# Kernel tuning notes

Hardware: AMD Instinct MI355X
Metric: run time of the kernel (lower is better)

## Reference

```python
import jax, jax.numpy as jnp
import numpy as np
import math

B, C, H, W = 4, 256, 64, 64
DQK = max(1, C // 8)  # 32


def setup_inputs() -> dict:
    key = jax.random.key(0)
    ks = jax.random.split(key, 6)
    x = jax.random.normal(ks[0], (B, C, H, W), dtype=jnp.float32)
    Wq = jax.random.normal(ks[1], (DQK, C), dtype=jnp.float32) * (1.0 / math.sqrt(C))
    bq = jnp.zeros((DQK,), dtype=jnp.float32)
    Wk = jax.random.normal(ks[2], (DQK, C), dtype=jnp.float32) * (1.0 / math.sqrt(C))
    bk = jnp.zeros((DQK,), dtype=jnp.float32)
    Wv = jax.random.normal(ks[3], (C, C), dtype=jnp.float32) * (1.0 / math.sqrt(C))
    bv = jnp.zeros((C,), dtype=jnp.float32)
    gamma = jax.random.normal(ks[4], (1,), dtype=jnp.float32)
    return {"x": x, "Wq": Wq, "bq": bq, "Wk": Wk, "bk": bk, "Wv": Wv, "bv": bv, "gamma": gamma}


def reference(x, Wq, bq, Wk, bk, Wv, bv, gamma):
    b, c, h, w = x.shape
    n = h * w
    xf = x.reshape(b, c, n)                                  # [B, C, N]
    # 1x1 convs == per-pixel linear projections
    q = jnp.einsum('bcn,dc->bdn', xf, Wq) + bq[None, :, None]  # [B, DQK, N]
    k = jnp.einsum('bcn,dc->bdn', xf, Wk) + bk[None, :, None]  # [B, DQK, N]
    v = jnp.einsum('bcn,oc->bon', xf, Wv) + bv[None, :, None]  # [B, C, N]
    scale = 1.0 / math.sqrt(q.shape[1] + 1e-8)
    attn = jnp.einsum('bdi,bdj->bij', q, k) * scale            # [B, N, N]
    attn = jax.nn.softmax(attn, axis=-1)
    out = jnp.einsum('bcj,bij->bci', v, attn)                  # [B, C, N]
    out = out.reshape(b, c, h, w)
    return gamma[0] * out + x
```

## Files before the change

kernel.cpp:

```cpp
#include <hip/hip_runtime.h>
#include <hip/hip_bf16.h>
#include <math.h>

#define BB   4
#define CC   256
#define DQK  32
#define NN   4096
#define QBLK 64
#define KVB  128
#define NQB  (NN / QBLK)
#define NTILES (NN / KVB)
#define SCALE 0.17677669529663687f

typedef short  bf16x8 __attribute__((ext_vector_type(8)));
typedef float  f32x4  __attribute__((ext_vector_type(4)));
typedef unsigned short u16;
typedef unsigned int   u32;

__device__ __forceinline__ u16 f2bf(float f) {
    __hip_bfloat16 h = __float2bfloat16(f);
    return *reinterpret_cast<u16*>(&h);
}

__global__ __launch_bounds__(256) void wprep_kernel(
    const float* __restrict__ Wq, const float* __restrict__ bq,
    const float* __restrict__ Wk, const float* __restrict__ bk,
    const float* __restrict__ Wv, const float* __restrict__ bv,
    u16* __restrict__ Wb, float* __restrict__ biasb)
{
    const int r = blockIdx.x;
    const int t = threadIdx.x;
    float w, bias;
    if (r < DQK)          { w = Wq[r * CC + t] * SCALE;     bias = bq[r] * SCALE; }
    else if (r < 2 * DQK) { w = Wk[(r - DQK) * CC + t];     bias = bk[r - DQK];  }
    else                  { w = Wv[(r - 2 * DQK) * CC + t]; bias = bv[r - 2 * DQK]; }
    Wb[r * CC + t] = f2bf(w);
    if (t == 0) biasb[r] = bias;
}

__global__ __launch_bounds__(512) void qkv_gemm(
    const float* __restrict__ x,
    const u16* __restrict__ Wb, const float* __restrict__ biasb,
    u16* __restrict__ qt, u16* __restrict__ kt, u16* __restrict__ v)
{
    __shared__ __align__(16) u16 xT[64][256];

    const int b   = blockIdx.y;
    const int n0  = blockIdx.x * 64;
    const int t   = threadIdx.x;

    {
        const int n_l = t & 63;
        const int cg  = t >> 6;
        const int sw  = (n_l & 15) << 3;
        #pragma unroll
        for (int p = 0; p < 8; ++p) {
            const int c0 = p * 32 + cg * 4;
            const float f0 = x[((size_t)b * CC + c0 + 0) * NN + n0 + n_l];
            const float f1 = x[((size_t)b * CC + c0 + 1) * NN + n0 + n_l];
            const float f2 = x[((size_t)b * CC + c0 + 2) * NN + n0 + n_l];
            const float f3 = x[((size_t)b * CC + c0 + 3) * NN + n0 + n_l];
            uint2 pk;
            pk.x = (u32)f2bf(f0) | ((u32)f2bf(f1) << 16);
            pk.y = (u32)f2bf(f2) | ((u32)f2bf(f3) << 16);
            *(uint2*)&xT[n_l][c0 ^ sw] = pk;
        }
    }
    __syncthreads();

    const int wid = t >> 6;
    const int mw  = wid & 3;
    const int nw  = wid >> 2;
    const int lane = t & 63;
    const int g    = lane >> 4;
    const int c16  = lane & 15;

    f32x4 acc[5][2];
    #pragma unroll
    for (int mf = 0; mf < 5; ++mf)
        #pragma unroll
        for (int nf = 0; nf < 2; ++nf)
            #pragma unroll
            for (int r = 0; r < 4; ++r) acc[mf][nf][r] = 0.f;

    const int rsw = c16 << 3;

    #pragma unroll
    for (int kk = 0; kk < 8; ++kk) {
        bf16x8 xf[2];
        #pragma unroll
        for (int nf = 0; nf < 2; ++nf)
            xf[nf] = *(const bf16x8*)&xT[nw * 32 + nf * 16 + c16][(kk * 32 + g * 8) ^ rsw];
        #pragma unroll
        for (int mf = 0; mf < 5; ++mf) {
            const bf16x8 wf = *(const bf16x8*)(Wb + (size_t)(mw * 80 + mf * 16 + c16) * CC + kk * 32 + g * 8);
            #pragma unroll
            for (int nf = 0; nf < 2; ++nf)
                acc[mf][nf] = __builtin_amdgcn_mfma_f32_16x16x32_bf16(wf, xf[nf], acc[mf][nf], 0, 0, 0);
        }
    }

    #pragma unroll
    for (int mf = 0; mf < 5; ++mf) {
        #pragma unroll
        for (int nf = 0; nf < 2; ++nf) {
            const int n = n0 + nw * 32 + nf * 16 + c16;
            #pragma unroll
            for (int r = 0; r < 4; ++r) {
                const int row = mw * 80 + mf * 16 + g * 4 + r;
                const float val = acc[mf][nf][r] + biasb[row];
                if (row < DQK)
                    qt[((size_t)b * NN + n) * DQK + row] = f2bf(val);
                else if (row < 2 * DQK)
                    kt[((size_t)b * NN + n) * DQK + (row - DQK)] = f2bf(val);
                else
                    v[((size_t)b * CC + (row - 2 * DQK)) * NN + n] = f2bf(val);
            }
        }
    }
}

__global__ __launch_bounds__(512, 2) void attn_kernel(
    const u16* __restrict__ qt, const u16* __restrict__ kt,
    const u16* __restrict__ vg,
    const float* __restrict__ x, const float* __restrict__ gamma_p,
    float* __restrict__ out)
{
    const int id   = blockIdx.x;
    const int xcd  = id & 7;
    const int b    = xcd >> 1;
    const int i0   = (((xcd & 1) << 5) + (id >> 3)) * QBLK;
    const int t    = threadIdx.x;
    const int wid  = t >> 6;
    const int lane = t & 63;
    const int g    = lane >> 4;
    const int c16  = lane & 15;
    const int jh   = wid >> 2;
    const int mw   = wid & 3;

    __shared__ __align__(16) u16 P_s[2][QBLK * KVB];
    __shared__ float l_s[2][QBLK];

    const u16* ktb = kt + (size_t)b * NN * DQK;
    const u16* vb  = vg + (size_t)b * CC * NN + (size_t)(wid * 32) * NN;

    const bf16x8 qa = *(const bf16x8*)(qt + ((size_t)b * NN + i0 + mw * 16 + c16) * DQK + g * 8);

    bf16x8 kb[4];
    #pragma unroll
    for (int jf = 0; jf < 4; ++jf)
        kb[jf] = *(const bf16x8*)(ktb + (size_t)(jh * 64 + jf * 16 + c16) * DQK + g * 8);

    f32x4 accv[2][4];
    #pragma unroll
    for (int cf = 0; cf < 2; ++cf)
        #pragma unroll
        for (int qf = 0; qf < 4; ++qf)
            #pragma unroll
            for (int r = 0; r < 4; ++r) accv[cf][qf][r] = 0.f;

    float l_acc = 0.f;

    for (int jt = 0; jt < NTILES; ++jt) {
        const int j0  = jt * KVB;
        const int buf = jt & 1;

        bf16x8 va[2][4];
        #pragma unroll
        for (int cf = 0; cf < 2; ++cf)
            #pragma unroll
            for (int ksl = 0; ksl < 4; ++ksl)
                va[cf][ksl] = *(const bf16x8*)(vb + (size_t)(cf * 16 + c16) * NN + j0 + ksl * 32 + g * 8);

        f32x4 sres[4];
        #pragma unroll
        for (int jf = 0; jf < 4; ++jf)
            sres[jf] = __builtin_amdgcn_mfma_f32_16x16x32_bf16(kb[jf], qa, (f32x4){0.f, 0.f, 0.f, 0.f}, 0, 0, 0);

        const int jn = ((jt + 1) & (NTILES - 1)) * KVB;
        #pragma unroll
        for (int jf = 0; jf < 4; ++jf)
            kb[jf] = *(const bf16x8*)(ktb + (size_t)(jn + jh * 64 + jf * 16 + c16) * DQK + g * 8);

        {
            const int rowbase = (mw * 16 + c16) * KVB;
            const int swz     = c16 << 3;
            #pragma unroll
            for (int jf = 0; jf < 4; ++jf) {
                const float p0 = __expf(sres[jf][0]);
                const float p1 = __expf(sres[jf][1]);
                const float p2 = __expf(sres[jf][2]);
                const float p3 = __expf(sres[jf][3]);
                l_acc += (p0 + p1) + (p2 + p3);
                u32 lo = (u32)f2bf(p0) | ((u32)f2bf(p1) << 16);
                u32 hi = (u32)f2bf(p2) | ((u32)f2bf(p3) << 16);
                uint2 pk; pk.x = lo; pk.y = hi;
                *(uint2*)&P_s[buf][rowbase + ((jh * 64 + jf * 16 + g * 4) ^ swz)] = pk;
            }
        }
        __syncthreads();

        __builtin_amdgcn_s_setprio(1);
        #pragma unroll
        for (int ksl = 0; ksl < 4; ++ksl) {
            #pragma unroll
            for (int qf = 0; qf < 4; ++qf) {
                const int row = c16 + 16 * qf;
                const int e   = (row * KVB + ksl * 32 + g * 8) ^ ((row & 15) << 3);
                const bf16x8 pb = *(const bf16x8*)&P_s[buf][e];
                #pragma unroll
                for (int cf = 0; cf < 2; ++cf)
                    accv[cf][qf] = __builtin_amdgcn_mfma_f32_16x16x32_bf16(va[cf][ksl], pb, accv[cf][qf], 0, 0, 0);
            }
        }
        __builtin_amdgcn_s_setprio(0);
    }

    l_acc += __shfl_xor(l_acc, 16);
    l_acc += __shfl_xor(l_acc, 32);
    if (lane < 16) l_s[jh][mw * 16 + c16] = l_acc;
    __syncthreads();

    const float gam = gamma_p[0];
    #pragma unroll
    for (int qf = 0; qf < 4; ++qf) {
        const int   qloc = c16 + 16 * qf;
        const int   qcol = i0 + qloc;
        const float linv = 1.0f / (l_s[0][qloc] + l_s[1][qloc]);
        #pragma unroll
        for (int cf = 0; cf < 2; ++cf) {
            #pragma unroll
            for (int r = 0; r < 4; ++r) {
                const int    c = wid * 32 + cf * 16 + g * 4 + r;
                const size_t o = ((size_t)b * CC + c) * NN + qcol;
                out[o] = gam * (accv[cf][qf][r] * linv) + x[o];
            }
        }
    }
}

extern "C" void kernel_launch(void* const* d_in, const int* in_sizes, int n_in,
                              void* d_out, int out_size, void* d_ws, size_t ws_size,
                              hipStream_t stream)
{
    const float* x     = (const float*)d_in[0];
    const float* Wq    = (const float*)d_in[1];
    const float* bq    = (const float*)d_in[2];
    const float* Wk    = (const float*)d_in[3];
    const float* bk    = (const float*)d_in[4];
    const float* Wv    = (const float*)d_in[5];
    const float* bv    = (const float*)d_in[6];
    const float* gamma = (const float*)d_in[7];
    float* out = (float*)d_out;

    u16* qt   = (u16*)d_ws;
    u16* kt   = qt + (size_t)BB * NN * DQK;
    u16* v    = kt + (size_t)BB * NN * DQK;
    u16* Wb   = v  + (size_t)BB * CC * NN;
    float* biasb = (float*)(Wb + 320 * CC);

    wprep_kernel<<<dim3(320), 256, 0, stream>>>(Wq, bq, Wk, bk, Wv, bv, Wb, biasb);
    qkv_gemm<<<dim3(NN / 64, BB), 512, 0, stream>>>(x, Wb, biasb, qt, kt, v);
    attn_kernel<<<dim3(BB * NQB), 512, 0, stream>>>(qt, kt, v, x, gamma, out);
}
```

Measured before the change: 105.9 us.

## Software-pipeline QK exp with previous tile's PV MFMAs to drop a barrier

Restructures the attention loop into a prologue, steady state and epilogue. Each iteration computes S and exp for tile jt into one P buffer while running the PV MFMAs on the previous tile's P from the other buffer. The exp/convert work is interleaved with the matrix ops per k-slice, and the loop needs only one __syncthreads per iteration instead of two phases. In exchange the code is longer and holds more live registers, and the last tile needs a separate drain step.

After: 118.4 us. 11.8% more time.

```diff
diff --git a/kernel.cpp b/kernel.cpp
--- a/kernel.cpp
+++ b/kernel.cpp
@@ -161,56 +161,96 @@
 
     float l_acc = 0.f;
 
-    for (int jt = 0; jt < NTILES; ++jt) {
-        const int j0  = jt * KVB;
-        const int buf = jt & 1;
-
-        bf16x8 va[2][4];
-        #pragma unroll
-        for (int cf = 0; cf < 2; ++cf)
-            #pragma unroll
-            for (int ksl = 0; ksl < 4; ++ksl)
-                va[cf][ksl] = *(const bf16x8*)(vb + (size_t)(cf * 16 + c16) * NN + j0 + ksl * 32 + g * 8);
-
+    const int rowbase = (mw * 16 + c16) * KVB;
+    const int swz     = c16 << 3;
+
+    {
         f32x4 sres[4];
         #pragma unroll
         for (int jf = 0; jf < 4; ++jf)
             sres[jf] = __builtin_amdgcn_mfma_f32_16x16x32_bf16(kb[jf], qa, (f32x4){0.f, 0.f, 0.f, 0.f}, 0, 0, 0);
+        #pragma unroll
+        for (int jf = 0; jf < 4; ++jf)
+            kb[jf] = *(const bf16x8*)(ktb + (size_t)(KVB + jh * 64 + jf * 16 + c16) * DQK + g * 8);
+        #pragma unroll
+        for (int i = 0; i < 4; ++i) {
+            const float p0 = __expf(sres[i][0]);
+            const float p1 = __expf(sres[i][1]);
+            const float p2 = __expf(sres[i][2]);
+            const float p3 = __expf(sres[i][3]);
+            l_acc += (p0 + p1) + (p2 + p3);
+            uint2 pk;
+            pk.x = (u32)f2bf(p0) | ((u32)f2bf(p1) << 16);
+            pk.y = (u32)f2bf(p2) | ((u32)f2bf(p3) << 16);
+            *(uint2*)&P_s[0][rowbase + ((jh * 64 + i * 16 + g * 4) ^ swz)] = pk;
+        }
+    }
+    __syncthreads();
+
+    for (int jt = 1; jt < NTILES; ++jt) {
+        const int j0   = jt * KVB;
+        const int buf  = jt & 1;
+        const int pbuf = buf ^ 1;
+        const int j0p  = j0 - KVB;
+
+        bf16x8 va[2][4];
+        #pragma unroll
+        for (int cf = 0; cf < 2; ++cf)
+            #pragma unroll
+            for (int ksl = 0; ksl < 4; ++ksl)
+                va[cf][ksl] = *(const bf16x8*)(vb + (size_t)(cf * 16 + c16) * NN + j0p + ksl * 32 + g * 8);
+
+        f32x4 sres[4];
+        #pragma unroll
+        for (int jf = 0; jf < 4; ++jf)
+            sres[jf] = __builtin_amdgcn_mfma_f32_16x16x32_bf16(kb[jf], qa, (f32x4){0.f, 0.f, 0.f, 0.f}, 0, 0, 0);
 
         const int jn = ((jt + 1) & (NTILES - 1)) * KVB;
         #pragma unroll
         for (int jf = 0; jf < 4; ++jf)
             kb[jf] = *(const bf16x8*)(ktb + (size_t)(jn + jh * 64 + jf * 16 + c16) * DQK + g * 8);
 
-        {
-            const int rowbase = (mw * 16 + c16) * KVB;
-            const int swz     = c16 << 3;
-            #pragma unroll
-            for (int jf = 0; jf < 4; ++jf) {
-                const float p0 = __expf(sres[jf][0]);
-                const float p1 = __expf(sres[jf][1]);
-                const float p2 = __expf(sres[jf][2]);
-                const float p3 = __expf(sres[jf][3]);
-                l_acc += (p0 + p1) + (p2 + p3);
-                u32 lo = (u32)f2bf(p0) | ((u32)f2bf(p1) << 16);
-                u32 hi = (u32)f2bf(p2) | ((u32)f2bf(p3) << 16);
-                uint2 pk; pk.x = lo; pk.y = hi;
-                *(uint2*)&P_s[buf][rowbase + ((jh * 64 + jf * 16 + g * 4) ^ swz)] = pk;
+        #pragma unroll
+        for (int i = 0; i < 4; ++i) {
+            const float p0 = __expf(sres[i][0]);
+            const float p1 = __expf(sres[i][1]);
+            const float p2 = __expf(sres[i][2]);
+            const float p3 = __expf(sres[i][3]);
+            l_acc += (p0 + p1) + (p2 + p3);
+            uint2 pk;
+            pk.x = (u32)f2bf(p0) | ((u32)f2bf(p1) << 16);
+            pk.y = (u32)f2bf(p2) | ((u32)f2bf(p3) << 16);
+            *(uint2*)&P_s[buf][rowbase + ((jh * 64 + i * 16 + g * 4) ^ swz)] = pk;
+
+            __builtin_amdgcn_s_setprio(1);
+            #pragma unroll
+            for (int qf = 0; qf < 4; ++qf) {
+                const int row = c16 + 16 * qf;
+                const int e   = (row * KVB + i * 32 + g * 8) ^ ((row & 15) << 3);
+                const bf16x8 pb = *(const bf16x8*)&P_s[pbuf][e];
+                accv[0][qf] = __builtin_amdgcn_mfma_f32_16x16x32_bf16(va[0][i], pb, accv[0][qf], 0, 0, 0);
+                accv[1][qf] = __builtin_amdgcn_mfma_f32_16x16x32_bf16(va[1][i], pb, accv[1][qf], 0, 0, 0);
             }
+            __builtin_amdgcn_s_setprio(0);
         }
         __syncthreads();
-
+    }
+
+    {
+        const int j0p  = (NTILES - 1) * KVB;
+        const int pbuf = (NTILES - 1) & 1;
         __builtin_amdgcn_s_setprio(1);
         #pragma unroll
         for (int ksl = 0; ksl < 4; ++ksl) {
+            const bf16x8 va0 = *(const bf16x8*)(vb + (size_t)(c16) * NN + j0p + ksl * 32 + g * 8);
+            const bf16x8 va1 = *(const bf16x8*)(vb + (size_t)(16 + c16) * NN + j0p + ksl * 32 + g * 8);
             #pragma unroll
             for (int qf = 0; qf < 4; ++qf) {
                 const int row = c16 + 16 * qf;
                 const int e   = (row * KVB + ksl * 32 + g * 8) ^ ((row & 15) << 3);
-                const bf16x8 pb = *(const bf16x8*)&P_s[buf][e];
-                #pragma unroll
-                for (int cf = 0; cf < 2; ++cf)
-                    accv[cf][qf] = __builtin_amdgcn_mfma_f32_16x16x32_bf16(va[cf][ksl], pb, accv[cf][qf], 0, 0, 0);
+                const bf16x8 pb = *(const bf16x8*)&P_s[pbuf][e];
+                accv[0][qf] = __builtin_amdgcn_mfma_f32_16x16x32_bf16(va0, pb, accv[0][qf], 0, 0, 0);
+                accv[1][qf] = __builtin_amdgcn_mfma_f32_16x16x32_bf16(va1, pb, accv[1][qf], 0, 0, 0);
             }
         }
         __builtin_amdgcn_s_setprio(0);
```
